# Performance work log

Measured on AMD Instinct MI355X. Metric: run time of the kernel, lower is better.

## Reference

```python
import jax, jax.numpy as jnp
import numpy as np

DATA = 2048   # data_size / hidden_size
WIDTH = 4096  # width_size
T = 1000      # len(ts)


def setup_inputs() -> dict:
    key = jax.random.key(0)
    ks = jax.random.split(key, 10)
    # ts: evenly spaced times; small dt keeps 1000 Euler steps stable
    ts = jnp.arange(T, dtype=jnp.float32) * 1e-3
    y0 = jax.random.normal(ks[0], (DATA,), dtype=jnp.float32)
    def lin(k, fan_out, fan_in):
        kw, kb = jax.random.split(k)
        s = 1.0 / np.sqrt(fan_in)
        W = jax.random.uniform(kw, (fan_out, fan_in), jnp.float32, -s, s)
        b = jax.random.uniform(kb, (fan_out,), jnp.float32, -s, s)
        return W, b
    # eqx.nn.MLP(depth=3): in->w, w->w, w->w, w->out, softplus on all but last
    W0, b0 = lin(ks[1], WIDTH, DATA)
    W1, b1 = lin(ks[2], WIDTH, WIDTH)
    W2, b2 = lin(ks[3], WIDTH, WIDTH)
    W3, b3 = lin(ks[4], DATA, WIDTH)
    return {"ts": ts, "y0": y0, "W0": W0, "b0": b0, "W1": W1, "b1": b1,
            "W2": W2, "b2": b2, "W3": W3, "b3": b3}


def reference(ts, y0, W0, b0, W1, b1, W2, b2, W3, b3):
    dt = ts[1] - ts[0]

    def mlp(y):
        h = jax.nn.softplus(W0 @ y + b0)
        h = jax.nn.softplus(W1 @ h + b1)
        h = jax.nn.softplus(W2 @ h + b2)
        return W3 @ h + b3

    def step(y, _):
        y1 = y + dt * mlp(y)  # Euler step: y + dt * f(t, y)
        return y1, y1

    _, ys = jax.lax.scan(step, y0, None, length=ts.shape[0])
    return ys  # [T, DATA]
```

## Files before the change

kernel.cpp:

```cpp
#include <hip/hip_runtime.h>

#define NWG   256
#define TPB_R 256
#define TPB_S 1024
#define NSTEP 1000
#define NDATA 2048
#define WIDTH 4096

typedef __attribute__((ext_vector_type(4))) float f32x4;
typedef __attribute__((ext_vector_type(2))) float f32x2;
typedef __attribute__((ext_vector_type(2))) unsigned int u32x2;
typedef __attribute__((ext_vector_type(4))) unsigned int u32x4;
typedef unsigned int uint;

#define SCHED_FENCE() __builtin_amdgcn_sched_barrier(0)


__device__ __forceinline__ float sp_f(float v) {
  return fmaxf(v, 0.0f) + log1pf(expf(-fabsf(v)));
}

__device__ __forceinline__ float wred(float v) {
#pragma unroll
  for (int m = 32; m > 0; m >>= 1) v += __shfl_xor(v, m, 64);
  return v;
}

__device__ __forceinline__ uint pk_bf16(float lo, float hi) {
  uint r;
  asm("v_cvt_pk_bf16_f32 %0, %1, %2" : "=v"(r) : "v"(lo), "v"(hi));
  return r;
}


__device__ __forceinline__ void wait_vm0()   { asm volatile("s_waitcnt vmcnt(0)" ::: "memory"); SCHED_FENCE(); }
template<int N>
__device__ __forceinline__ void wait_vmN()   { asm volatile("s_waitcnt vmcnt(%0)" :: "n"(N) : "memory"); SCHED_FENCE(); }
__device__ __forceinline__ void wait_lgkm0() { asm volatile("s_waitcnt lgkmcnt(0)" ::: "memory"); SCHED_FENCE(); }
__device__ __forceinline__ void wgbar()      { __builtin_amdgcn_s_barrier(); SCHED_FENCE(); }


__device__ __forceinline__ void st_sc_x1(float* p, float v) {
  asm volatile("global_store_dword %0, %1, off sc0 sc1" :: "v"(p), "v"(v) : "memory");
}
__device__ __forceinline__ void st_sc_x2(float* p, f32x2 v) {
  asm volatile("global_store_dwordx2 %0, %1, off sc0 sc1" :: "v"(p), "v"(v) : "memory");
}
__device__ __forceinline__ void st_sc_u2(uint* p, u32x2 v) {
  asm volatile("global_store_dwordx2 %0, %1, off sc0 sc1" :: "v"(p), "v"(v) : "memory");
}
__device__ __forceinline__ void ld_sc_x2_issue(const float* p, f32x2& v) {
  asm volatile("global_load_dwordx2 %0, %1, off sc0 sc1" : "=v"(v) : "v"(p) : "memory");
}
__device__ __forceinline__ void ld_sc_x4_issue(const f32x4* p, f32x4& v) {
  asm volatile("global_load_dwordx4 %0, %1, off sc0 sc1" : "=v"(v) : "v"(p) : "memory");
}
__device__ __forceinline__ void ld_sc_u4_issue(const u32x4* p, u32x4& v) {
  asm volatile("global_load_dwordx4 %0, %1, off sc0 sc1" : "=v"(v) : "v"(p) : "memory");
}
__device__ __forceinline__ void ld_sc_x1_issue(const float* p, float& v) {
  asm volatile("global_load_dword %0, %1, off sc0 sc1" : "=v"(v) : "v"(p) : "memory");
}
__device__ __forceinline__ uint ld_sc_u32(const uint* p) {
  uint v;
  asm volatile("global_load_dword %0, %1, off sc0 sc1\n\ts_waitcnt vmcnt(0)"
               : "=v"(v) : "v"(p) : "memory");
  return v;
}
__device__ __forceinline__ void st_sc_u32(uint* p, uint v) {
  asm volatile("global_store_dword %0, %1, off sc0 sc1" :: "v"(p), "v"(v) : "memory");
}
__device__ __forceinline__ void ld_g(const u32x4* p, u32x4& v) {
  asm volatile("global_load_dwordx4 %0, %1, off" : "=v"(v) : "v"(p) : "memory");
}


__device__ __forceinline__ void sync_stage_h(uint* flags, uint tag, int wg,
                                             int tid, const uint* src,
                                             uint* xs) {
  wgbar();
  if (tid == 0) st_sc_u32(flags + wg * 16, tag);
  const uint* fp = flags + tid * 16;
  if (ld_sc_u32(fp) < tag) {
    do { __builtin_amdgcn_s_sleep(1); } while (ld_sc_u32(fp) < tag);
  }
  const u32x4* s = (const u32x4*)src + tid * 2;
  u32x4 a, b;
  ld_sc_u4_issue(s + 0, a); ld_sc_u4_issue(s + 1, b);
  wait_vm0();
  u32x4* l = (u32x4*)xs + tid * 2;
  l[0] = a; l[1] = b;
  wait_lgkm0();
  wgbar();
}

__device__ __forceinline__ void sync_stage_y(uint* flags, uint tag, int wg,
                                             int tid, const float* src,
                                             uint* xs) {
  wgbar();
  if (tid == 0) st_sc_u32(flags + wg * 16, tag);
  const uint* fp = flags + tid * 16;
  if (ld_sc_u32(fp) < tag) {
    do { __builtin_amdgcn_s_sleep(1); } while (ld_sc_u32(fp) < tag);
  }
  const f32x4* s = (const f32x4*)src + tid * 2;
  f32x4 a, b;
  ld_sc_x4_issue(s + 0, a); ld_sc_x4_issue(s + 1, b);
  wait_vm0();
  u32x4 o;
  o.x = pk_bf16(a.x, a.y); o.y = pk_bf16(a.z, a.w);
  o.z = pk_bf16(b.x, b.y); o.w = pk_bf16(b.z, b.w);
  ((u32x4*)xs)[tid] = o;
  wait_lgkm0();
  wgbar();
}

__device__ __forceinline__ void stage_plain_2048(const float* src, uint* xs, int tid) {
  wgbar();
  const f32x4* s = (const f32x4*)src + tid * 2;
  f32x4 a = s[0], b = s[1];
  u32x4 o;
  o.x = pk_bf16(a.x, a.y); o.y = pk_bf16(a.z, a.w);
  o.z = pk_bf16(b.x, b.y); o.w = pk_bf16(b.z, b.w);
  ((u32x4*)xs)[tid] = o;
  wait_lgkm0();
  wgbar();
}


__device__ __forceinline__ uint bfr(float f) {
  uint u = __float_as_uint(f);
  return (u + 0x7fffu + ((u >> 16) & 1u)) >> 16;
}

__global__ void cvt_perm(const float* __restrict__ in, u32x4* __restrict__ out,
                         int rows, int K) {
  int idx = blockIdx.x * 256 + threadIdx.x;
  int cpr = K >> 3;
  if (idx >= rows * cpr) return;
  int row = idx / cpr, c = idx - row * cpr;
  int j = c >> 6, lane = c & 63;
  const f32x4* p = (const f32x4*)(in + (size_t)row * K + j * 512 + lane * 4);
  f32x4 lo = p[0];
  f32x4 hi = p[64];
  u32x4 o;
  o.x = bfr(lo.x) | (bfr(lo.y) << 16);
  o.y = bfr(lo.z) | (bfr(lo.w) << 16);
  o.z = bfr(hi.x) | (bfr(hi.y) << 16);
  o.w = bfr(hi.z) | (bfr(hi.w) << 16);
  out[idx] = o;
}


__global__ void __launch_bounds__(256) gemm_G(const float* __restrict__ W0,
                                              const float* __restrict__ W3,
                                              uint* __restrict__ Gp) {
  __shared__ float As[64][33];
  __shared__ float Bs[32][65];
  const int bid = blockIdx.x;
  const int tr = bid >> 6, tc = bid & 63;
  const int r0 = tr * 64, c0 = tc * 64;
  const int tid = threadIdx.x;
  float acc[4][4] = {};
  for (int kb = 0; kb < 2048; kb += 32) {
    {
      int row = tid >> 2, kk = (tid & 3) * 8;
      const float* src = W0 + (size_t)(r0 + row) * 2048 + kb + kk;
#pragma unroll
      for (int i = 0; i < 8; ++i) As[row][kk + i] = src[i];
    }
    {
      int k = tid >> 3, cc = (tid & 7) * 8;
      const float* src = W3 + (size_t)(kb + k) * 4096 + c0 + cc;
#pragma unroll
      for (int i = 0; i < 8; ++i) Bs[k][cc + i] = src[i];
    }
    __syncthreads();
    const int rr = (tid >> 4) * 4, cc = (tid & 15) * 4;
#pragma unroll
    for (int k = 0; k < 32; ++k) {
      float a0 = As[rr + 0][k], a1 = As[rr + 1][k], a2 = As[rr + 2][k], a3 = As[rr + 3][k];
      float bx0 = Bs[k][cc + 0], bx1 = Bs[k][cc + 1], bx2 = Bs[k][cc + 2], bx3 = Bs[k][cc + 3];
      acc[0][0] = fmaf(a0, bx0, acc[0][0]); acc[0][1] = fmaf(a0, bx1, acc[0][1]);
      acc[0][2] = fmaf(a0, bx2, acc[0][2]); acc[0][3] = fmaf(a0, bx3, acc[0][3]);
      acc[1][0] = fmaf(a1, bx0, acc[1][0]); acc[1][1] = fmaf(a1, bx1, acc[1][1]);
      acc[1][2] = fmaf(a1, bx2, acc[1][2]); acc[1][3] = fmaf(a1, bx3, acc[1][3]);
      acc[2][0] = fmaf(a2, bx0, acc[2][0]); acc[2][1] = fmaf(a2, bx1, acc[2][1]);
      acc[2][2] = fmaf(a2, bx2, acc[2][2]); acc[2][3] = fmaf(a2, bx3, acc[2][3]);
      acc[3][0] = fmaf(a3, bx0, acc[3][0]); acc[3][1] = fmaf(a3, bx1, acc[3][1]);
      acc[3][2] = fmaf(a3, bx2, acc[3][2]); acc[3][3] = fmaf(a3, bx3, acc[3][3]);
    }
    __syncthreads();
  }
  const int rr = (tid >> 4) * 4, cc = (tid & 15) * 4;
#pragma unroll
  for (int i = 0; i < 4; ++i) {
    int r = r0 + rr + i;
    int c = c0 + cc;
    int j = c >> 9, q = c & 511;
    int lane, w;
    if (q < 256) { lane = q >> 2; w = 0; } else { lane = (q - 256) >> 2; w = 2; }
    uint* dst = Gp + ((size_t)r * 512 + (size_t)j * 64 + lane) * 4 + w;
    u32x2 v;
    v.x = bfr(acc[i][0]) | (bfr(acc[i][1]) << 16);
    v.y = bfr(acc[i][2]) | (bfr(acc[i][3]) << 16);
    *(u32x2*)dst = v;
  }
}


#define VD(W, X, s) asm("v_dot2_f32_bf16 %0, %1, %2, %0" : "+v"(s) : "v"(W), "v"(X))

#define QF(Q, s) do{                                                 \
  VD((Q).x, xa2.x, s); VD((Q).y, xa2.y, s);                          \
  VD((Q).z, xb2.x, s); VD((Q).w, xb2.y, s);                          \
}while(0)

#define DC(Q, j, s) do{                                              \
  u32x2 xa2 = xw2[(j)*128 + lane];                                   \
  u32x2 xb2 = xw2[(j)*128 + 64 + lane];                              \
  QF(Q, s);                                                          \
}while(0)

#define DL4(j) do{                                                   \
  u32x2 xa2 = xw2[(j)*128 + lane];                                   \
  u32x2 xb2 = xw2[(j)*128 + 64 + lane];                              \
  u32x4 Q0 = w1p[0*512 + (j)*64 + lane];                             \
  u32x4 Q1 = w1p[1*512 + (j)*64 + lane];                             \
  u32x4 Q2 = w1p[2*512 + (j)*64 + lane];                             \
  u32x4 Q3 = w1p[3*512 + (j)*64 + lane];                             \
  QF(Q0, s0); QF(Q1, s1); QF(Q2, s2); QF(Q3, s3);                    \
}while(0)

#define DR4(j, Qa, Qb, Qc, Qd) do{                                   \
  u32x2 xa2 = xw2[(j)*128 + lane];                                   \
  u32x2 xb2 = xw2[(j)*128 + 64 + lane];                              \
  QF(Qa, s0); QF(Qb, s1); QF(Qc, s2); QF(Qd, s3);                    \
}while(0)

#define DR2(j, Qa, Qb) do{                                           \
  u32x2 xa2 = xw2[(j)*128 + lane];                                   \
  u32x2 xb2 = xw2[(j)*128 + 64 + lane];                              \
  QF(Qa, s0); QF(Qb, s1);                                            \
}while(0)

#define SREG(x) __int_as_float(__builtin_amdgcn_readfirstlane(__float_as_int(x)))


__global__ void __launch_bounds__(TPB_R, 1) ode_fused(
    const float* __restrict__ ts, const float* __restrict__ y0,
    const u32x4* __restrict__ W0p, const float* __restrict__ b0,
    const u32x4* __restrict__ W1p, const float* __restrict__ b1,
    const u32x4* __restrict__ W2p, const float* __restrict__ b2,
    const u32x4* __restrict__ W3p, const float* __restrict__ b3,
    const u32x4* __restrict__ Gp,
    float* __restrict__ out, uint* x1buf, uint* h1buf, uint* h2buf,
    uint* flags)
{
  __shared__ u32x4 W1lds[16 * 512];
  __shared__ uint xs[2048];
  const int wg = blockIdx.x, tid = threadIdx.x;
  const int wave = tid >> 6, lane = tid & 63;
  const float dt = ts[1] - ts[0];
  const int rw = wg * 16 + wave * 4;
  const int rf = wg * 8 + wave * 2;
  const u32x2* xw2 = (const u32x2*)xs;
  const u32x4* w1p = &W1lds[(wave * 4) * 512];

#pragma unroll
  for (int k = 0; k < 32; ++k)
    W1lds[k * 256 + tid] = W1p[(size_t)wg * 8192 + k * 256 + tid];

#define L2W(r,j) W2p[(size_t)(rw+(r))*512 + (j)*64 + lane]
  u32x4 C00=L2W(0,0),C01=L2W(0,1),C02=L2W(0,2),C03=L2W(0,3),C04=L2W(0,4),C05=L2W(0,5),C06=L2W(0,6),C07=L2W(0,7);
  u32x4 C10=L2W(1,0),C11=L2W(1,1),C12=L2W(1,2),C13=L2W(1,3),C14=L2W(1,4),C15=L2W(1,5),C16=L2W(1,6),C17=L2W(1,7);
  u32x4 C20=L2W(2,0),C21=L2W(2,1),C22=L2W(2,2),C23=L2W(2,3),C24=L2W(2,4),C25=L2W(2,5),C26=L2W(2,6),C27=L2W(2,7);
  u32x4 C30=L2W(3,0),C31=L2W(3,1),C32=L2W(3,2),C33=L2W(3,3),C34=L2W(3,4),C35=L2W(3,5),C36=L2W(3,6),C37=L2W(3,7);
#define L3W(r,j) W3p[(size_t)(rf+(r))*512 + (j)*64 + lane]
  u32x4 D00=L3W(0,0),D01=L3W(0,1),D02=L3W(0,2),D03=L3W(0,3),D04=L3W(0,4),D05=L3W(0,5),D06=L3W(0,6),D07=L3W(0,7);
  u32x4 D10=L3W(1,0),D11=L3W(1,1),D12=L3W(1,2),D13=L3W(1,3),D14=L3W(1,4),D15=L3W(1,5),D16=L3W(1,6),D17=L3W(1,7);

  const float b00=SREG(b0[rw]), b01=SREG(b0[rw+1]), b02=SREG(b0[rw+2]), b03=SREG(b0[rw+3]);
  const float b10=SREG(b1[rw]), b11=SREG(b1[rw+1]), b12=SREG(b1[rw+2]), b13=SREG(b1[rw+3]);
  const float b20=SREG(b2[rw]), b21=SREG(b2[rw+1]), b22=SREG(b2[rw+2]), b23=SREG(b2[rw+3]);
  const float b30=SREG(b3[rf]), b31=SREG(b3[rf+1]);

  wait_vm0(); wait_lgkm0();
  wgbar();

  u32x4 F00,F01,F02,F03,F04,F05,F06,F07, F10,F11,F12,F13,F14,F15,F16,F17;
#define ISSW0ALL() do{                                                         \
  const u32x4* p0_ = W0p + (size_t)(rw+0)*256 + lane;                          \
  const u32x4* p1_ = W0p + (size_t)(rw+1)*256 + lane;                          \
  const u32x4* p2_ = W0p + (size_t)(rw+2)*256 + lane;                          \
  const u32x4* p3_ = W0p + (size_t)(rw+3)*256 + lane;                          \
  ld_g(p0_,F00); ld_g(p0_+64,F01); ld_g(p0_+128,F02); ld_g(p0_+192,F03);       \
  ld_g(p1_,F04); ld_g(p1_+64,F05); ld_g(p1_+128,F06); ld_g(p1_+192,F07);       \
  ld_g(p2_,F10); ld_g(p2_+64,F11); ld_g(p2_+128,F12); ld_g(p2_+192,F13);       \
  ld_g(p3_,F14); ld_g(p3_+64,F15); ld_g(p3_+128,F16); ld_g(p3_+192,F17);       \
}while(0)

  float c0, c1, c2, c3, u0, u1, u2, u3;
  stage_plain_2048(b3, xs, tid);
  ISSW0ALL(); wait_vm0();
  c0=0.f; DC(F00,0,c0); DC(F01,1,c0); DC(F02,2,c0); DC(F03,3,c0);
  c1=0.f; DC(F04,0,c1); DC(F05,1,c1); DC(F06,2,c1); DC(F07,3,c1);
  c2=0.f; DC(F10,0,c2); DC(F11,1,c2); DC(F12,2,c2); DC(F13,3,c2);
  c3=0.f; DC(F14,0,c3); DC(F15,1,c3); DC(F16,2,c3); DC(F17,3,c3);
  c0 = wred(c0); c1 = wred(c1); c2 = wred(c2); c3 = wred(c3);

  stage_plain_2048(y0, xs, tid);
  ISSW0ALL(); wait_vm0();
  u0=0.f; DC(F00,0,u0); DC(F01,1,u0); DC(F02,2,u0); DC(F03,3,u0);
  u1=0.f; DC(F04,0,u1); DC(F05,1,u1); DC(F06,2,u1); DC(F07,3,u1);
  u2=0.f; DC(F10,0,u2); DC(F11,1,u2); DC(F12,2,u2); DC(F13,3,u2);
  u3=0.f; DC(F14,0,u3); DC(F15,1,u3); DC(F16,2,u3); DC(F17,3,u3);
  u0 = wred(u0); u1 = wred(u1); u2 = wred(u2); u3 = wred(u3);

  float yv0 = y0[rf], yv1 = y0[rf + 1];

  if (lane == 0) {
    u32x2 xv;
    xv.x = pk_bf16(sp_f(u0 + b00), sp_f(u1 + b01));
    xv.y = pk_bf16(sp_f(u2 + b02), sp_f(u3 + b03));
    st_sc_u2(x1buf + (rw >> 1), xv);
  }
  wait_vm0();

#define ISSG(r, Q0,Q1,Q2,Q3,Q4,Q5,Q6,Q7) do{                                   \
  const u32x4* p_ = Gp + (size_t)(rw+(r))*512 + lane;                          \
  ld_g(p_,Q0); ld_g(p_+64,Q1); ld_g(p_+128,Q2); ld_g(p_+192,Q3);               \
  ld_g(p_+256,Q4); ld_g(p_+320,Q5); ld_g(p_+384,Q6); ld_g(p_+448,Q7);          \
}while(0)

  uint tag = 1;
  for (int step = 0; step < NSTEP; ++step) {
    float s0, s1, s2, s3;
    sync_stage_h(flags, tag, wg, tid, x1buf, xs); ++tag;
    s0=0.f; s1=0.f; s2=0.f; s3=0.f;
    DL4(0); DL4(1); DL4(2); DL4(3); DL4(4); DL4(5); DL4(6); DL4(7);
    s0 = wred(s0); s1 = wred(s1); s2 = wred(s2); s3 = wred(s3);
    if (lane == 0) {
      u32x2 v; v.x = pk_bf16(sp_f(s0+b10), sp_f(s1+b11));
               v.y = pk_bf16(sp_f(s2+b12), sp_f(s3+b13));
      st_sc_u2(h1buf + (rw >> 1), v);
    }
    wait_vm0();

    sync_stage_h(flags, tag, wg, tid, h1buf, xs); ++tag;
    s0=0.f; s1=0.f; s2=0.f; s3=0.f;
    DR4(0, C00, C10, C20, C30); DR4(1, C01, C11, C21, C31);
    DR4(2, C02, C12, C22, C32); DR4(3, C03, C13, C23, C33);
    DR4(4, C04, C14, C24, C34); DR4(5, C05, C15, C25, C35);
    DR4(6, C06, C16, C26, C36); DR4(7, C07, C17, C27, C37);
    s0 = wred(s0); s1 = wred(s1); s2 = wred(s2); s3 = wred(s3);
    if (lane == 0) {
      u32x2 v; v.x = pk_bf16(sp_f(s0+b20), sp_f(s1+b21));
               v.y = pk_bf16(sp_f(s2+b22), sp_f(s3+b23));
      st_sc_u2(h2buf + (rw >> 1), v);
    }
    wait_vm0();

    ISSG(0, F00,F01,F02,F03,F04,F05,F06,F07);
    ISSG(1, F10,F11,F12,F13,F14,F15,F16,F17);

    sync_stage_h(flags, tag, wg, tid, h2buf, xs); ++tag;
    float g0=0.f, g1=0.f, g2=0.f, g3=0.f;
    DC(F00,0,g0); DC(F01,1,g0); DC(F02,2,g0); DC(F03,3,g0);
    DC(F04,4,g0); DC(F05,5,g0); DC(F06,6,g0); DC(F07,7,g0);
    DC(F10,0,g1); DC(F11,1,g1); DC(F12,2,g1); DC(F13,3,g1);
    DC(F14,4,g1); DC(F15,5,g1); DC(F16,6,g1); DC(F17,7,g1);
    ISSG(2, F00,F01,F02,F03,F04,F05,F06,F07);
    ISSG(3, F10,F11,F12,F13,F14,F15,F16,F17);
    s0=0.f; s1=0.f;
    DR2(0, D00, D10); DR2(1, D01, D11); DR2(2, D02, D12); DR2(3, D03, D13);
    DR2(4, D04, D14); DR2(5, D05, D15); DR2(6, D06, D16); DR2(7, D07, D17);
    wait_vm0();
    DC(F00,0,g2); DC(F01,1,g2); DC(F02,2,g2); DC(F03,3,g2);
    DC(F04,4,g2); DC(F05,5,g2); DC(F06,6,g2); DC(F07,7,g2);
    DC(F10,0,g3); DC(F11,1,g3); DC(F12,2,g3); DC(F13,3,g3);
    DC(F14,4,g3); DC(F15,5,g3); DC(F16,6,g3); DC(F17,7,g3);
    g0 = wred(g0); g1 = wred(g1); g2 = wred(g2); g3 = wred(g3);
    s0 = wred(s0); s1 = wred(s1);
    u0 += dt * (g0 + c0); u1 += dt * (g1 + c1);
    u2 += dt * (g2 + c2); u3 += dt * (g3 + c3);
    yv0 += dt * (s0 + b30); yv1 += dt * (s1 + b31);
    float* yout = out + (size_t)step * NDATA;
    if (lane == 0) {
      f32x2 yv; yv.x = yv0; yv.y = yv1;
      st_sc_x2(yout + rf, yv);
      u32x2 xv;
      xv.x = pk_bf16(sp_f(u0 + b00), sp_f(u1 + b01));
      xv.y = pk_bf16(sp_f(u2 + b02), sp_f(u3 + b03));
      st_sc_u2(x1buf + (rw >> 1), xv);
    }
    wait_vm0();
  }
}


__global__ void __launch_bounds__(TPB_R, 1) ode_res(
    const float* __restrict__ ts, const float* __restrict__ y0,
    const u32x4* __restrict__ W0p, const float* __restrict__ b0,
    const u32x4* __restrict__ W1p, const float* __restrict__ b1,
    const u32x4* __restrict__ W2p, const float* __restrict__ b2,
    const u32x4* __restrict__ W3p, const float* __restrict__ b3,
    float* __restrict__ out, uint* hA, uint* hB,
    uint* flags)
{
  __shared__ u32x4 W1lds[16 * 512];
  __shared__ uint xs[2048];
  const int wg = blockIdx.x, tid = threadIdx.x;
  const int wave = tid >> 6, lane = tid & 63;
  const float dt = ts[1] - ts[0];
  const int rw = wg * 16 + wave * 4;
  const int rf = wg * 8 + wave * 2;
  const u32x2* xw2 = (const u32x2*)xs;
  const u32x4* w1p = &W1lds[(wave * 4) * 512];

#pragma unroll
  for (int k = 0; k < 32; ++k)
    W1lds[k * 256 + tid] = W1p[(size_t)wg * 8192 + k * 256 + tid];

  u32x4 C00=L2W(0,0),C01=L2W(0,1),C02=L2W(0,2),C03=L2W(0,3),C04=L2W(0,4),C05=L2W(0,5),C06=L2W(0,6),C07=L2W(0,7);
  u32x4 C10=L2W(1,0),C11=L2W(1,1),C12=L2W(1,2),C13=L2W(1,3),C14=L2W(1,4),C15=L2W(1,5),C16=L2W(1,6),C17=L2W(1,7);
  u32x4 C20=L2W(2,0),C21=L2W(2,1),C22=L2W(2,2),C23=L2W(2,3),C24=L2W(2,4),C25=L2W(2,5),C26=L2W(2,6),C27=L2W(2,7);
  u32x4 C30=L2W(3,0),C31=L2W(3,1),C32=L2W(3,2),C33=L2W(3,3),C34=L2W(3,4),C35=L2W(3,5),C36=L2W(3,6),C37=L2W(3,7);
  u32x4 D00=L3W(0,0),D01=L3W(0,1),D02=L3W(0,2),D03=L3W(0,3),D04=L3W(0,4),D05=L3W(0,5),D06=L3W(0,6),D07=L3W(0,7);
  u32x4 D10=L3W(1,0),D11=L3W(1,1),D12=L3W(1,2),D13=L3W(1,3),D14=L3W(1,4),D15=L3W(1,5),D16=L3W(1,6),D17=L3W(1,7);

  const float b00=SREG(b0[rw]), b01=SREG(b0[rw+1]), b02=SREG(b0[rw+2]), b03=SREG(b0[rw+3]);
  const float b10=SREG(b1[rw]), b11=SREG(b1[rw+1]), b12=SREG(b1[rw+2]), b13=SREG(b1[rw+3]);
  const float b20=SREG(b2[rw]), b21=SREG(b2[rw+1]), b22=SREG(b2[rw+2]), b23=SREG(b2[rw+3]);
  const float b30=SREG(b3[rf]), b31=SREG(b3[rf+1]);

  wait_vm0(); wait_lgkm0();
  wgbar();

  const u32x4* w0base = W0p + (size_t)rw * 256 + lane;
#define ISSW0(r, Qa, Qb, Qc, Qd) do{ const u32x4* p_ = w0base + (size_t)(r)*256; \
  ld_g(p_, Qa); ld_g(p_+64, Qb); ld_g(p_+128, Qc); ld_g(p_+192, Qd); }while(0)

  u32x4 E0a,E0b,E0c,E0d, E1a,E1b,E1c,E1d, E2a,E2b,E2c,E2d, E3a,E3b,E3c,E3d;
  ISSW0(0, E0a,E0b,E0c,E0d);

  uint tag = 0;
  const float* yin = y0;
  for (int step = 0; step < NSTEP; ++step) {
    float s0, s1, s2, s3;
    sync_stage_y(flags, tag, wg, tid, yin, xs); ++tag;
    ISSW0(1, E1a,E1b,E1c,E1d);
    s0 = 0.f; DC(E0a,0,s0); DC(E0b,1,s0); DC(E0c,2,s0); DC(E0d,3,s0);
    ISSW0(2, E2a,E2b,E2c,E2d);
    wait_vmN<4>();
    s1 = 0.f; DC(E1a,0,s1); DC(E1b,1,s1); DC(E1c,2,s1); DC(E1d,3,s1);
    ISSW0(3, E3a,E3b,E3c,E3d);
    wait_vmN<4>();
    s2 = 0.f; DC(E2a,0,s2); DC(E2b,1,s2); DC(E2c,2,s2); DC(E2d,3,s2);
    wait_vm0();
    s3 = 0.f; DC(E3a,0,s3); DC(E3b,1,s3); DC(E3c,2,s3); DC(E3d,3,s3);
    s0 = wred(s0); s1 = wred(s1); s2 = wred(s2); s3 = wred(s3);
    if (lane == 0) {
      u32x2 v; v.x = pk_bf16(sp_f(s0+b00), sp_f(s1+b01));
               v.y = pk_bf16(sp_f(s2+b02), sp_f(s3+b03));
      st_sc_u2(hA + (rw >> 1), v);
    }
    wait_vm0();

    sync_stage_h(flags, tag, wg, tid, hA, xs); ++tag;
    s0=0.f; s1=0.f; s2=0.f; s3=0.f;
    DL4(0); DL4(1); DL4(2); DL4(3); DL4(4); DL4(5); DL4(6); DL4(7);
    s0 = wred(s0); s1 = wred(s1); s2 = wred(s2); s3 = wred(s3);
    if (lane == 0) {
      u32x2 v; v.x = pk_bf16(sp_f(s0+b10), sp_f(s1+b11));
               v.y = pk_bf16(sp_f(s2+b12), sp_f(s3+b13));
      st_sc_u2(hB + (rw >> 1), v);
    }
    wait_vm0();

    sync_stage_h(flags, tag, wg, tid, hB, xs); ++tag;
    s0=0.f; s1=0.f; s2=0.f; s3=0.f;
    DR4(0, C00, C10, C20, C30); DR4(1, C01, C11, C21, C31);
    DR4(2, C02, C12, C22, C32); DR4(3, C03, C13, C23, C33);
    DR4(4, C04, C14, C24, C34); DR4(5, C05, C15, C25, C35);
    DR4(6, C06, C16, C26, C36); DR4(7, C07, C17, C27, C37);
    s0 = wred(s0); s1 = wred(s1); s2 = wred(s2); s3 = wred(s3);
    if (lane == 0) {
      u32x2 v; v.x = pk_bf16(sp_f(s0+b20), sp_f(s1+b21));
               v.y = pk_bf16(sp_f(s2+b22), sp_f(s3+b23));
      st_sc_u2(hA + (rw >> 1), v);
    }
    wait_vm0();

    sync_stage_h(flags, tag, wg, tid, hA, xs); ++tag;
    f32x2 yo;
    ld_sc_x2_issue(yin + rf, yo);
    s0=0.f; s1=0.f;
    DR2(0, D00, D10); DR2(1, D01, D11); DR2(2, D02, D12); DR2(3, D03, D13);
    DR2(4, D04, D14); DR2(5, D05, D15); DR2(6, D06, D16); DR2(7, D07, D17);
    s0 = wred(s0); s1 = wred(s1);
    wait_vm0();
    float* yout = out + (size_t)step * NDATA;
    if (lane == 0) {
      f32x2 v; v.x = yo.x + dt * (s0 + b30); v.y = yo.y + dt * (s1 + b31);
      st_sc_x2(yout + rf, v);
    }
    ISSW0(0, E0a,E0b,E0c,E0d);
    wait_vmN<4>();
    yin = yout;
  }
}


__device__ __forceinline__ void gbar1k(uint* flags, uint tag, int wg, int tid) {
  wgbar();
  if (tid == 0) st_sc_u32(flags + wg * 16, tag);
  if (tid < NWG) {
    const uint* fp = flags + tid * 16;
    if (ld_sc_u32(fp) < tag) {
      do { __builtin_amdgcn_s_sleep(1); } while (ld_sc_u32(fp) < tag);
    }
  }
  wgbar();
}

__device__ __forceinline__ void stage4096_1k(const float* src, float* xsf, int tid) {
  f32x4 a;
  ld_sc_x4_issue((const f32x4*)src + tid, a);
  wait_vm0();
  ((f32x4*)xsf)[tid] = a;
  wait_lgkm0();
  wgbar();
}
__device__ __forceinline__ void stage2048_1k(const float* src, float* xsf, int tid) {
  f32x4 a;
  bool act = tid < 512;
  if (act) ld_sc_x4_issue((const f32x4*)src + tid, a);
  wait_vm0();
  if (act) ((f32x4*)xsf)[tid] = a;
  wait_lgkm0();
  wgbar();
}

__device__ __forceinline__ void issue_row_f32(const float* W, size_t elemidx, int lane, f32x4* wr, int ni) {
  const f32x4* p = (const f32x4*)(W + elemidx) + lane;
  for (int i = 0; i < ni; ++i)
    asm volatile("global_load_dwordx4 %0, %1, off" : "=v"(wr[i]) : "v"(p + i * 64) : "memory");
}

template<int NI>
__device__ __forceinline__ float dot_row_f32(const f32x4* wr, const float* xsf, int xoff, int lane) {
  const f32x4* x4 = (const f32x4*)xsf + xoff;
  float a = 0.f;
#pragma unroll
  for (int i = 0; i < NI; ++i) {
    f32x4 xv = x4[i * 64 + lane];
    a = fmaf(wr[i].x, xv.x, a); a = fmaf(wr[i].y, xv.y, a);
    a = fmaf(wr[i].z, xv.z, a); a = fmaf(wr[i].w, xv.w, a);
  }
  return a;
}

__global__ void __launch_bounds__(TPB_S, 1) ode_stream(
    const float* __restrict__ ts, const float* __restrict__ y0,
    const float* __restrict__ W0, const float* __restrict__ b0,
    const float* __restrict__ W1, const float* __restrict__ b1,
    const float* __restrict__ W2, const float* __restrict__ b2,
    const float* __restrict__ W3, const float* __restrict__ b3,
    float* __restrict__ out, float* hA, float* hB,
    uint* flags)
{
  __shared__ float xsf[WIDTH];
  __shared__ float ps[16];
  const int wg = blockIdx.x, tid = threadIdx.x;
  const int wave = tid >> 6, lane = tid & 63;
  const float dt = ts[1] - ts[0];
  const int rw = wg * 16 + wave;
  const int rF = wg * 8 + (wave >> 1);
  const int hf = wave & 1;

  f32x4 w0r[8], w1r[16], w2r[16], w3r[8];
  issue_row_f32(W0, (size_t)rw * NDATA, lane, w0r, 8);

  uint tag = 0;
  const float* yin = y0;
  for (int step = 0; step < NSTEP; ++step) {
    stage2048_1k(yin, xsf, tid);
    float a = wred(dot_row_f32<8>(w0r, xsf, 0, lane));
    if (lane == 0) st_sc_x1(hA + rw, sp_f(a + b0[rw]));
    issue_row_f32(W1, (size_t)rw * WIDTH, lane, w1r, 16);
    wait_vmN<16>();
    gbar1k(flags, ++tag, wg, tid);

    stage4096_1k(hA, xsf, tid);
    a = wred(dot_row_f32<16>(w1r, xsf, 0, lane));
    if (lane == 0) st_sc_x1(hB + rw, sp_f(a + b1[rw]));
    issue_row_f32(W2, (size_t)rw * WIDTH, lane, w2r, 16);
    wait_vmN<16>();
    gbar1k(flags, ++tag, wg, tid);

    stage4096_1k(hB, xsf, tid);
    a = wred(dot_row_f32<16>(w2r, xsf, 0, lane));
    if (lane == 0) st_sc_x1(hA + rw, sp_f(a + b2[rw]));
    issue_row_f32(W3, (size_t)rF * WIDTH + (size_t)hf * 2048, lane, w3r, 8);
    wait_vmN<8>();
    gbar1k(flags, ++tag, wg, tid);

    stage4096_1k(hA, xsf, tid);
    float yo;
    ld_sc_x1_issue(yin + rF, yo);
    a = wred(dot_row_f32<8>(w3r, xsf, hf * 512, lane));
    if (lane == 0) ps[wave] = a;
    wait_lgkm0();
    wgbar();
    wait_vm0();
    float* yout = out + (size_t)step * NDATA;
    if (hf == 0 && lane == 0) {
      float tot = ps[wave] + ps[wave + 1];
      st_sc_x1(yout + rF, yo + dt * (tot + b3[rF]));
    }
    issue_row_f32(W0, (size_t)rw * NDATA, lane, w0r, 8);
    wait_vmN<8>();
    gbar1k(flags, ++tag, wg, tid);
    yin = yout;
  }
}


#define WS_X1   0
#define WS_H1   8192
#define WS_H2   16384
#define WS_CNT  32768
#define WS_WB   65536
static const size_t N_W0 = (size_t)WIDTH * NDATA;
static const size_t N_W1 = (size_t)WIDTH * WIDTH;
static const size_t N_W3 = (size_t)NDATA * WIDTH;
static const size_t N_G  = (size_t)WIDTH * WIDTH;

extern "C" void kernel_launch(void* const* d_in, const int* in_sizes, int n_in,
                              void* d_out, int out_size, void* d_ws, size_t ws_size,
                              hipStream_t stream) {
  const float* ts = (const float*)d_in[0];
  const float* y0 = (const float*)d_in[1];
  const float* W0 = (const float*)d_in[2];
  const float* b0 = (const float*)d_in[3];
  const float* W1 = (const float*)d_in[4];
  const float* b1 = (const float*)d_in[5];
  const float* W2 = (const float*)d_in[6];
  const float* b2 = (const float*)d_in[7];
  const float* W3 = (const float*)d_in[8];
  const float* b3 = (const float*)d_in[9];
  float* out = (float*)d_out;

  char* ws = (char*)d_ws;
  uint* flags = (uint*)(ws + WS_CNT);

  hipMemsetAsync(ws + WS_CNT, 0, 16384, stream);

  const size_t need_bf  = WS_WB + (N_W0 + 2 * N_W1 + N_W3) * 2;
  const size_t need_fus = need_bf + N_G * 2;

  u32x4* W0p = (u32x4*)(ws + WS_WB);
  u32x4* W1p = W0p + N_W0 / 8;
  u32x4* W2p = W1p + N_W1 / 8;
  u32x4* W3p = W2p + N_W1 / 8;
  u32x4* Gp  = W3p + N_W3 / 8;

  if (ws_size >= need_fus) {
    hipLaunchKernelGGL(cvt_perm, dim3((unsigned)(N_W0 / 8 / 256)), dim3(256), 0, stream, W0, W0p, WIDTH, NDATA);
    hipLaunchKernelGGL(cvt_perm, dim3((unsigned)(N_W1 / 8 / 256)), dim3(256), 0, stream, W1, W1p, WIDTH, WIDTH);
    hipLaunchKernelGGL(cvt_perm, dim3((unsigned)(N_W1 / 8 / 256)), dim3(256), 0, stream, W2, W2p, WIDTH, WIDTH);
    hipLaunchKernelGGL(cvt_perm, dim3((unsigned)(N_W3 / 8 / 256)), dim3(256), 0, stream, W3, W3p, NDATA, WIDTH);
    hipLaunchKernelGGL(gemm_G, dim3(4096), dim3(256), 0, stream, W0, W3, (uint*)Gp);
    uint* x1b = (uint*)(ws + WS_X1);
    uint* h1b = (uint*)(ws + WS_H1);
    uint* h2b = (uint*)(ws + WS_H2);
    hipLaunchKernelGGL(ode_fused, dim3(NWG), dim3(TPB_R), 0, stream,
                       ts, y0, W0p, b0, W1p, b1, W2p, b2, W3p, b3, Gp,
                       out, x1b, h1b, h2b, flags);
  } else if (ws_size >= need_bf) {
    hipLaunchKernelGGL(cvt_perm, dim3((unsigned)(N_W0 / 8 / 256)), dim3(256), 0, stream, W0, W0p, WIDTH, NDATA);
    hipLaunchKernelGGL(cvt_perm, dim3((unsigned)(N_W1 / 8 / 256)), dim3(256), 0, stream, W1, W1p, WIDTH, WIDTH);
    hipLaunchKernelGGL(cvt_perm, dim3((unsigned)(N_W1 / 8 / 256)), dim3(256), 0, stream, W2, W2p, WIDTH, WIDTH);
    hipLaunchKernelGGL(cvt_perm, dim3((unsigned)(N_W3 / 8 / 256)), dim3(256), 0, stream, W3, W3p, NDATA, WIDTH);
    uint* hA = (uint*)(ws + WS_X1);
    uint* hB = (uint*)(ws + WS_H2);
    hipLaunchKernelGGL(ode_res, dim3(NWG), dim3(TPB_R), 0, stream,
                       ts, y0, W0p, b0, W1p, b1, W2p, b2, W3p, b3,
                       out, hA, hB, flags);
  } else {
    float* hAf = (float*)(ws + WS_X1);
    float* hBf = (float*)(ws + WS_H2);
    hipLaunchKernelGGL(ode_stream, dim3(NWG), dim3(TPB_S), 0, stream,
                       ts, y0, W0, b0, W1, b1, W2, b2, W3, b3,
                       out, hAf, hBf, flags);
  }
}
```

Before: 19.87 ms.

## Rewrite W0·W3 precompute GEMM with bf16 dot2 and larger 128x64 tiles

The one-time G = W0·W3 product moves from an fp32 FMA kernel with 64x64 tiles to a kernel that packs operands into bf16 pairs in shared memory and accumulates with v_dot2_f32_bf16. Each thread now computes an 8x4 tile, and vectorized f32x4 global loads plus u32x4 LDS reads replace scalar accesses. This cuts both arithmetic and memory traffic in a setup GEMM of about 17 GFLOP that runs before the ODE loop. The trade-off is that G is accumulated from bf16-rounded inputs rather than fp32, which changes numerics slightly even though the output was already stored as bf16.

```diff
diff --git a/kernel.cpp b/kernel.cpp
--- a/kernel.cpp
+++ b/kernel.cpp
@@ -152,51 +152,59 @@
 }
 
 
-__global__ void __launch_bounds__(256) gemm_G(const float* __restrict__ W0,
-                                              const float* __restrict__ W3,
-                                              uint* __restrict__ Gp) {
-  __shared__ float As[64][33];
-  __shared__ float Bs[32][65];
+#define VD(W, X, s) asm("v_dot2_f32_bf16 %0, %1, %2, %0" : "+v"(s) : "v"(W), "v"(X))
+
+
+__global__ void __launch_bounds__(256) gemm_G2(const float* __restrict__ W0,
+                                               const float* __restrict__ W3,
+                                               uint* __restrict__ Gp) {
+  __shared__ uint As[16][128];
+  __shared__ uint Bs[16][64];
   const int bid = blockIdx.x;
-  const int tr = bid >> 6, tc = bid & 63;
-  const int r0 = tr * 64, c0 = tc * 64;
+  const int tm = bid >> 6, tn = bid & 63;
+  const int r0 = tm * 128, c0 = tn * 64;
   const int tid = threadIdx.x;
-  float acc[4][4] = {};
+  const int m0 = (tid >> 4) * 8, n0 = (tid & 15) * 4;
+  float acc[8][4] = {};
   for (int kb = 0; kb < 2048; kb += 32) {
+    __syncthreads();
     {
-      int row = tid >> 2, kk = (tid & 3) * 8;
-      const float* src = W0 + (size_t)(r0 + row) * 2048 + kb + kk;
+      int row = tid >> 1, ks = (tid & 1) * 16;
+      const f32x4* src = (const f32x4*)(W0 + (size_t)(r0 + row) * 2048 + kb + ks);
+      f32x4 v0 = src[0], v1 = src[1], v2 = src[2], v3 = src[3];
+      int kp = ks >> 1;
+      As[kp + 0][row] = pk_bf16(v0.x, v0.y); As[kp + 1][row] = pk_bf16(v0.z, v0.w);
+      As[kp + 2][row] = pk_bf16(v1.x, v1.y); As[kp + 3][row] = pk_bf16(v1.z, v1.w);
+      As[kp + 4][row] = pk_bf16(v2.x, v2.y); As[kp + 5][row] = pk_bf16(v2.z, v2.w);
+      As[kp + 6][row] = pk_bf16(v3.x, v3.y); As[kp + 7][row] = pk_bf16(v3.z, v3.w);
+    }
+    {
+      int kp = tid >> 4, nn = (tid & 15) * 4;
+      const f32x4* s0 = (const f32x4*)(W3 + (size_t)(kb + 2 * kp) * 4096 + c0 + nn);
+      const f32x4* s1 = (const f32x4*)(W3 + (size_t)(kb + 2 * kp + 1) * 4096 + c0 + nn);
+      f32x4 a = s0[0], b = s1[0];
+      Bs[kp][nn + 0] = pk_bf16(a.x, b.x);
+      Bs[kp][nn + 1] = pk_bf16(a.y, b.y);
+      Bs[kp][nn + 2] = pk_bf16(a.z, b.z);
+      Bs[kp][nn + 3] = pk_bf16(a.w, b.w);
+    }
+    __syncthreads();
+#define G4(av, r) do{ VD(av, bq.x, acc[r][0]); VD(av, bq.y, acc[r][1]); \
+                      VD(av, bq.z, acc[r][2]); VD(av, bq.w, acc[r][3]); }while(0)
 #pragma unroll
-      for (int i = 0; i < 8; ++i) As[row][kk + i] = src[i];
-    }
-    {
-      int k = tid >> 3, cc = (tid & 7) * 8;
-      const float* src = W3 + (size_t)(kb + k) * 4096 + c0 + cc;
+    for (int kp = 0; kp < 16; ++kp) {
+      u32x4 a0 = *(const u32x4*)&As[kp][m0];
+      u32x4 a1 = *(const u32x4*)&As[kp][m0 + 4];
+      u32x4 bq = *(const u32x4*)&Bs[kp][n0];
+      G4(a0.x, 0); G4(a0.y, 1); G4(a0.z, 2); G4(a0.w, 3);
+      G4(a1.x, 4); G4(a1.y, 5); G4(a1.z, 6); G4(a1.w, 7);
+    }
+#undef G4
+  }
 #pragma unroll
-      for (int i = 0; i < 8; ++i) Bs[k][cc + i] = src[i];
-    }
-    __syncthreads();
-    const int rr = (tid >> 4) * 4, cc = (tid & 15) * 4;
-#pragma unroll
-    for (int k = 0; k < 32; ++k) {
-      float a0 = As[rr + 0][k], a1 = As[rr + 1][k], a2 = As[rr + 2][k], a3 = As[rr + 3][k];
-      float bx0 = Bs[k][cc + 0], bx1 = Bs[k][cc + 1], bx2 = Bs[k][cc + 2], bx3 = Bs[k][cc + 3];
-      acc[0][0] = fmaf(a0, bx0, acc[0][0]); acc[0][1] = fmaf(a0, bx1, acc[0][1]);
-      acc[0][2] = fmaf(a0, bx2, acc[0][2]); acc[0][3] = fmaf(a0, bx3, acc[0][3]);
-      acc[1][0] = fmaf(a1, bx0, acc[1][0]); acc[1][1] = fmaf(a1, bx1, acc[1][1]);
-      acc[1][2] = fmaf(a1, bx2, acc[1][2]); acc[1][3] = fmaf(a1, bx3, acc[1][3]);
-      acc[2][0] = fmaf(a2, bx0, acc[2][0]); acc[2][1] = fmaf(a2, bx1, acc[2][1]);
-      acc[2][2] = fmaf(a2, bx2, acc[2][2]); acc[2][3] = fmaf(a2, bx3, acc[2][3]);
-      acc[3][0] = fmaf(a3, bx0, acc[3][0]); acc[3][1] = fmaf(a3, bx1, acc[3][1]);
-      acc[3][2] = fmaf(a3, bx2, acc[3][2]); acc[3][3] = fmaf(a3, bx3, acc[3][3]);
-    }
-    __syncthreads();
-  }
-  const int rr = (tid >> 4) * 4, cc = (tid & 15) * 4;
-#pragma unroll
-  for (int i = 0; i < 4; ++i) {
-    int r = r0 + rr + i;
-    int c = c0 + cc;
+  for (int i = 0; i < 8; ++i) {
+    int r = r0 + m0 + i;
+    int c = c0 + n0;
     int j = c >> 9, q = c & 511;
     int lane, w;
     if (q < 256) { lane = q >> 2; w = 0; } else { lane = (q - 256) >> 2; w = 2; }
@@ -208,8 +216,6 @@
   }
 }
 
-
-#define VD(W, X, s) asm("v_dot2_f32_bf16 %0, %1, %2, %0" : "+v"(s) : "v"(W), "v"(X))
 
 #define QF(Q, s) do{                                                 \
   VD((Q).x, xa2.x, s); VD((Q).y, xa2.y, s);                          \
@@ -671,7 +677,7 @@
     hipLaunchKernelGGL(cvt_perm, dim3((unsigned)(N_W1 / 8 / 256)), dim3(256), 0, stream, W1, W1p, WIDTH, WIDTH);
     hipLaunchKernelGGL(cvt_perm, dim3((unsigned)(N_W1 / 8 / 256)), dim3(256), 0, stream, W2, W2p, WIDTH, WIDTH);
     hipLaunchKernelGGL(cvt_perm, dim3((unsigned)(N_W3 / 8 / 256)), dim3(256), 0, stream, W3, W3p, NDATA, WIDTH);
-    hipLaunchKernelGGL(gemm_G, dim3(4096), dim3(256), 0, stream, W0, W3, (uint*)Gp);
+    hipLaunchKernelGGL(gemm_G2, dim3(2048), dim3(256), 0, stream, W0, W3, (uint*)Gp);
     uint* x1b = (uint*)(ws + WS_X1);
     uint* h1b = (uint*)(ws + WS_H1);
     uint* h2b = (uint*)(ws + WS_H2);
```

Result: faster. 18.73 ms, median of 2 (-5.8%).
